# Kernel optimization log

Measured on AMD Instinct MI355X. Metric: run time of the kernel, lower is better.

Reference implementation:

```python
import jax, jax.numpy as jnp
import numpy as np

B, L, S, DIM, NH = 4, 1024, 1024, 1024, 16
DH = DIM // NH


def setup_inputs() -> dict:
    key = jax.random.key(0)
    ks = jax.random.split(key, 16)
    std = 0.02
    inp = {
        'q': jax.random.normal(ks[0], (B, L, DIM), jnp.float32),
        'k': jax.random.normal(ks[1], (B, S, DIM), jnp.float32),
        'v': jax.random.normal(ks[2], (B, S, DIM), jnp.float32),
        'attn_mask': jax.random.bernoulli(ks[3], 0.9, (B, L, S)),
        'pos_bias': jax.random.normal(ks[4], (B, NH, L, S), jnp.float32),
        'Wq': jax.random.normal(ks[5], (DIM, DIM), jnp.float32) * std,
        'bq': jnp.zeros((DIM,), jnp.float32),
        'Wk': jax.random.normal(ks[6], (DIM, DIM), jnp.float32) * std,
        'bk': jnp.zeros((DIM,), jnp.float32),
        'Wv': jax.random.normal(ks[7], (DIM, DIM), jnp.float32) * std,
        'bv': jnp.zeros((DIM,), jnp.float32),
        'Wp': jax.random.normal(ks[8], (DIM, DIM), jnp.float32) * std,
        'bp': jnp.zeros((DIM,), jnp.float32),
        'is_causal': 1,
    }
    return inp


def _attention(q, k, v, attn_mask, pos_bias, Wq, bq, Wk, bk, Wv, bv, Wp, bp, is_causal):
    b, l, _ = q.shape
    s = k.shape[1]
    qh = (q @ Wq + bq).reshape(b, l, NH, DH)   # (B,L,nH,dh)
    kh = (k @ Wk + bk).reshape(b, s, NH, DH)
    vh = (v @ Wv + bv).reshape(b, s, NH, DH)

    mask = attn_mask  # (B,L,S) bool
    if is_causal:
        causal = jnp.tril(jnp.ones((l, l), dtype=bool))
        causal = jnp.pad(causal, ((0, 0), (s - l, 0)), constant_values=True)  # (L,S)
        mask = mask & causal[None]
    # rows with no allowed key attend everywhere (matches torch row-fix)
    row_any = mask.any(axis=-1, keepdims=True)
    mask = jnp.where(row_any, mask, True)

    bias = jnp.where(mask[:, None, :, :], pos_bias, -jnp.inf)  # (B,nH,L,S)
    scale = 1.0 / np.sqrt(DH).astype(np.float32)
    scores = jnp.einsum('blhd,bshd->bhls', qh, kh) * scale + bias
    attn = jax.nn.softmax(scores, axis=-1)
    o = jnp.einsum('bhls,bshd->blhd', attn, vh).reshape(b, l, NH * DH)
    return o @ Wp + bp


def reference(q, k, v, attn_mask, pos_bias, Wq, bq, Wk, bk, Wv, bv, Wp, bp, is_causal):
    return _attention(q, k, v, attn_mask, pos_bias, Wq, bq, Wk, bk, Wv, bv, Wp, bp, is_causal)
```

## Files before the change

kernel.cpp:

```cpp
#include <hip/hip_runtime.h>
#include <hip/hip_bf16.h>

typedef __hip_bfloat16 bf16;
typedef __attribute__((ext_vector_type(4))) float  floatx4;
typedef __attribute__((ext_vector_type(8))) short  short8;
typedef __attribute__((ext_vector_type(8))) __bf16 bf16x8;

constexpr int Bc = 4, Lc = 1024, Sc = 1024, DIMc = 1024, NHc = 16, DHc = 64;

template <typename V>
__device__ auto mfma_bf16_sel(V a, V b, floatx4 c, int)
    -> decltype(__builtin_amdgcn_mfma_f32_16x16x32_bf16(a, b, c, 0, 0, 0)) {
  return __builtin_amdgcn_mfma_f32_16x16x32_bf16(a, b, c, 0, 0, 0);
}
template <typename V>
__device__ floatx4 mfma_bf16_sel(V a, V b, floatx4 c, long) {
  bf16x8 a2 = __builtin_bit_cast(bf16x8, a);
  bf16x8 b2 = __builtin_bit_cast(bf16x8, b);
  return __builtin_amdgcn_mfma_f32_16x16x32_bf16(a2, b2, c, 0, 0, 0);
}
__device__ inline floatx4 mfma_bf16(short8 a, short8 b, floatx4 c) {
  return mfma_bf16_sel(a, b, c, 0);
}

union U8 { uint4 u; bf16 h[8]; };

__device__ inline U8 cvt8(float4 f0, float4 f1) {
    U8 t;
    t.h[0] = __float2bfloat16(f0.x); t.h[1] = __float2bfloat16(f0.y);
    t.h[2] = __float2bfloat16(f0.z); t.h[3] = __float2bfloat16(f0.w);
    t.h[4] = __float2bfloat16(f1.x); t.h[5] = __float2bfloat16(f1.y);
    t.h[6] = __float2bfloat16(f1.z); t.h[7] = __float2bfloat16(f1.w);
    return t;
}

__global__ __launch_bounds__(256)
void prep_kernel(const float* __restrict__ Wq, const float* __restrict__ Wk,
                 const float* __restrict__ Wv, const float* __restrict__ Wp,
                 const int* __restrict__ mask, const int* __restrict__ is_causal_p,
                 bf16* __restrict__ wqt, bf16* __restrict__ wkt,
                 bf16* __restrict__ wvt, bf16* __restrict__ wpt,
                 unsigned long long* __restrict__ mbits,
                 int* __restrict__ rowany_g)
{
    __shared__ float tile[64][68];
    const int tid = threadIdx.x;
    int blk = blockIdx.x;

    if (blk < 1024) {
        const int w  = blk >> 8, t2 = blk & 255;
        const float* W  = (w == 0) ? Wq : (w == 1) ? Wk : (w == 2) ? Wv : Wp;
        bf16*        Wt = (w == 0) ? wqt : (w == 1) ? wkt : (w == 2) ? wvt : wpt;
        const int tk = (t2 >> 4) << 6;
        const int tn = (t2 & 15) << 6;
        #pragma unroll
        for (int i = 0; i < 4; ++i) {
            const int r = (tid >> 4) + i * 16;
            const int c = (tid & 15) << 2;
            *(float4*)(&tile[r][c]) =
                *(const float4*)(W + (size_t)(tk + r) * DIMc + tn + c);
        }
        __syncthreads();
        #pragma unroll
        for (int j = 0; j < 2; ++j) {
            const int nn = tid >> 2;
            const int kc = (tid & 3) + j * 4;
            U8 o;
            #pragma unroll
            for (int u = 0; u < 8; ++u)
                o.h[u] = __float2bfloat16(tile[kc * 8 + u][nn]);
            *(uint4*)(Wt + (size_t)(tn + nn) * DIMc + tk + kc * 8) = o.u;
        }
    } else {
        const int mb  = blk - 1024;
        const int rIb = tid >> 4;
        const int w   = tid & 15;
        const int row = mb * 16 + rIb;
        const int l   = row & (Lc - 1);
        const bool causal = (is_causal_p[0] != 0);

        const int4* mr4 = (const int4*)(mask + (size_t)row * Sc + w * 64);
        unsigned long long bits = 0ull;
        #pragma unroll
        for (int i = 0; i < 16; ++i) {
            int4 m4 = mr4[i];
            unsigned long long nib =
                (unsigned long long)((m4.x != 0) | ((m4.y != 0) << 1) |
                                     ((m4.z != 0) << 2) | ((m4.w != 0) << 3));
            bits |= nib << (4 * i);
        }
        mbits[(size_t)row * 16 + w] = bits;

        const int limit = causal ? l : (Sc - 1);
        const int base  = w * 64;
        unsigned long long am;
        if (limit >= base + 63)  am = bits;
        else if (limit < base)   am = 0ull;
        else                     am = bits & ((2ull << (limit - base)) - 1ull);
        unsigned long long red = am;
        #pragma unroll
        for (int d2 = 1; d2 < 16; d2 <<= 1) red |= __shfl_xor(red, d2);
        if (w == 0) rowany_g[row] = (red != 0ull) ? 1 : 0;
    }
}

constexpr int GPAD = 72;

__global__ __launch_bounds__(256)
void gemm_qkv_kernel(const float* __restrict__ q, const float* __restrict__ k,
                     const float* __restrict__ v,
                     const bf16* __restrict__ wqt, const bf16* __restrict__ wkt,
                     const bf16* __restrict__ wvt,
                     const float* __restrict__ bq, const float* __restrict__ bk,
                     const float* __restrict__ bv,
                     bf16* __restrict__ qh, bf16* __restrict__ kh,
                     bf16* __restrict__ vt)
{
    __shared__ bf16 As[128 * GPAD];
    __shared__ bf16 Bs[128 * GPAD];

    const int z = blockIdx.z;
    const float* A    = (z == 0) ? q   : (z == 1) ? k   : v;
    const bf16*  Bt   = (z == 0) ? wqt : (z == 1) ? wkt : wvt;
    const float* bias = (z == 0) ? bq  : (z == 1) ? bk  : bv;
    bf16*        out  = (z == 0) ? qh  : (z == 1) ? kh  : vt;

    const int tid  = threadIdx.x;
    const int wave = tid >> 6;
    const int lane = tid & 63;
    const int n = lane & 15, g = lane >> 4;
    const int m0 = blockIdx.x * 128;
    const int n0 = blockIdx.y * 128;
    const int wq_m = (wave & 1) * 64, wq_n = (wave >> 1) * 64;

    floatx4 acc[4][4];
    #pragma unroll
    for (int a = 0; a < 4; ++a)
        #pragma unroll
        for (int b2 = 0; b2 < 4; ++b2)
            acc[a][b2] = (floatx4){0.f, 0.f, 0.f, 0.f};

    const int srow   = tid >> 3;
    const int schunk = (tid & 7) * 8;

    float4 a0[4], a1[4]; uint4 bR[4];
    #pragma unroll
    for (int i = 0; i < 4; ++i) {
        const float* ap = A + (size_t)(m0 + srow + i * 32) * DIMc + schunk;
        a0[i] = ((const float4*)ap)[0];
        a1[i] = ((const float4*)ap)[1];
        bR[i] = *(const uint4*)(Bt + (size_t)(n0 + srow + i * 32) * DIMc + schunk);
    }

    for (int k0 = 0; k0 < DIMc; k0 += 64) {
        __syncthreads();
        #pragma unroll
        for (int i = 0; i < 4; ++i) {
            const int r = srow + i * 32;
            U8 t = cvt8(a0[i], a1[i]);
            *(uint4*)(&As[r * GPAD + schunk]) = t.u;
            *(uint4*)(&Bs[r * GPAD + schunk]) = bR[i];
        }
        __syncthreads();
        if (k0 + 64 < DIMc) {
            #pragma unroll
            for (int i = 0; i < 4; ++i) {
                const float* ap =
                    A + (size_t)(m0 + srow + i * 32) * DIMc + k0 + 64 + schunk;
                a0[i] = ((const float4*)ap)[0];
                a1[i] = ((const float4*)ap)[1];
                bR[i] = *(const uint4*)(Bt + (size_t)(n0 + srow + i * 32) * DIMc +
                                        k0 + 64 + schunk);
            }
        }
        #pragma unroll
        for (int ks = 0; ks < 2; ++ks) {
            short8 af[4], bf_[4];
            #pragma unroll
            for (int t = 0; t < 4; ++t) {
                af[t]  = *(const short8*)(&As[(wq_m + t * 16 + n) * GPAD + ks * 32 + g * 8]);
                bf_[t] = *(const short8*)(&Bs[(wq_n + t * 16 + n) * GPAD + ks * 32 + g * 8]);
            }
            #pragma unroll
            for (int tm = 0; tm < 4; ++tm)
                #pragma unroll
                for (int tn = 0; tn < 4; ++tn)
                    acc[tm][tn] = mfma_bf16(af[tm], bf_[tn], acc[tm][tn]);
        }
    }

    #pragma unroll
    for (int tn = 0; tn < 4; ++tn) {
        const int col = n0 + wq_n + tn * 16 + n;
        const float bval = bias[col];
        #pragma unroll
        for (int tm = 0; tm < 4; ++tm) {
            #pragma unroll
            for (int r = 0; r < 4; ++r) {
                const int row = m0 + wq_m + tm * 16 + g * 4 + r;
                const float vv = acc[tm][tn][r] + bval;
                const int bb = row >> 10, ll = row & (Lc - 1);
                const int hh = col >> 6,  dd = col & 63;
                size_t idx;
                if (z < 2) idx = (((size_t)(bb * NHc + hh) * Lc + ll) * DHc) + dd;
                else       idx = (((size_t)(bb * NHc + hh) * DHc + dd) * Sc) + ll;
                out[idx] = __float2bfloat16(vv);
            }
        }
    }
}

__global__ __launch_bounds__(256)
void gemm_out_kernel(const bf16* __restrict__ A, const bf16* __restrict__ Bt,
                     const float* __restrict__ bias, float* __restrict__ out)
{
    __shared__ bf16 As[128 * GPAD];
    __shared__ bf16 Bs[128 * GPAD];

    const int tid  = threadIdx.x;
    const int wave = tid >> 6;
    const int lane = tid & 63;
    const int n = lane & 15, g = lane >> 4;
    const int m0 = blockIdx.x * 128;
    const int n0 = blockIdx.y * 128;
    const int wq_m = (wave & 1) * 64, wq_n = (wave >> 1) * 64;

    floatx4 acc[4][4];
    #pragma unroll
    for (int a = 0; a < 4; ++a)
        #pragma unroll
        for (int b2 = 0; b2 < 4; ++b2)
            acc[a][b2] = (floatx4){0.f, 0.f, 0.f, 0.f};

    const int srow   = tid >> 3;
    const int schunk = (tid & 7) * 8;

    uint4 aR[4], bR[4];
    #pragma unroll
    for (int i = 0; i < 4; ++i) {
        aR[i] = *(const uint4*)(A  + (size_t)(m0 + srow + i * 32) * DIMc + schunk);
        bR[i] = *(const uint4*)(Bt + (size_t)(n0 + srow + i * 32) * DIMc + schunk);
    }

    for (int k0 = 0; k0 < DIMc; k0 += 64) {
        __syncthreads();
        #pragma unroll
        for (int i = 0; i < 4; ++i) {
            const int r = srow + i * 32;
            *(uint4*)(&As[r * GPAD + schunk]) = aR[i];
            *(uint4*)(&Bs[r * GPAD + schunk]) = bR[i];
        }
        __syncthreads();
        if (k0 + 64 < DIMc) {
            #pragma unroll
            for (int i = 0; i < 4; ++i) {
                aR[i] = *(const uint4*)(A  + (size_t)(m0 + srow + i * 32) * DIMc +
                                        k0 + 64 + schunk);
                bR[i] = *(const uint4*)(Bt + (size_t)(n0 + srow + i * 32) * DIMc +
                                        k0 + 64 + schunk);
            }
        }
        #pragma unroll
        for (int ks = 0; ks < 2; ++ks) {
            short8 af[4], bf_[4];
            #pragma unroll
            for (int t = 0; t < 4; ++t) {
                af[t]  = *(const short8*)(&As[(wq_m + t * 16 + n) * GPAD + ks * 32 + g * 8]);
                bf_[t] = *(const short8*)(&Bs[(wq_n + t * 16 + n) * GPAD + ks * 32 + g * 8]);
            }
            #pragma unroll
            for (int tm = 0; tm < 4; ++tm)
                #pragma unroll
                for (int tn = 0; tn < 4; ++tn)
                    acc[tm][tn] = mfma_bf16(af[tm], bf_[tn], acc[tm][tn]);
        }
    }

    #pragma unroll
    for (int tn = 0; tn < 4; ++tn) {
        const int col = n0 + wq_n + tn * 16 + n;
        const float bval = bias[col];
        #pragma unroll
        for (int tm = 0; tm < 4; ++tm) {
            #pragma unroll
            for (int r = 0; r < 4; ++r) {
                const int row = m0 + wq_m + tm * 16 + g * 4 + r;
                out[(size_t)row * DIMc + col] = acc[tm][tn][r] + bval;
            }
        }
    }
}

constexpr int PADk = 72;

__global__ __launch_bounds__(256)
void flash_attn_kernel(const bf16* __restrict__ qh, const bf16* __restrict__ kh,
                       const bf16* __restrict__ vt,
                       const unsigned long long* __restrict__ mbits,
                       const int* __restrict__ rowany_g,
                       const float* __restrict__ pos_bias,
                       const int* __restrict__ is_causal_p, bf16* __restrict__ o)
{
    __shared__ bf16 Ks[64 * PADk];
    __shared__ bf16 Vs[64 * PADk];
    __shared__ bf16 Pw[4][16 * PADk];
    __shared__ int rowany[64];
    __shared__ int hasfix_s;

    const int tid  = threadIdx.x;
    const int lane = tid & 63;
    const int wave = tid >> 6;
    const int n = lane & 15;
    const int g = lane >> 4;

    const int qt = 15 - (blockIdx.x >> 6);
    const int bh = blockIdx.x & 63;
    const int h  = bh & (NHc - 1);
    const int b  = bh >> 4;
    const int l0 = qt * 64;
    const bool causal = (is_causal_p[0] != 0);

    if (tid == 0) hasfix_s = 0;
    __syncthreads();
    if (tid < 64) {
        const int ra = rowany_g[(b << 10) + l0 + tid];
        rowany[tid] = ra;
        if (ra == 0) atomicOr(&hasfix_s, 1);
    }
    __syncthreads();
    const bool hasfix = (hasfix_s != 0);

    const int qrow_frag = l0 + wave * 16 + n;
    const bf16* qp = qh + ((size_t)bh * Lc + qrow_frag) * DHc;
    const short8 qf0 = *(const short8*)(qp + g * 8);
    const short8 qf1 = *(const short8*)(qp + 32 + g * 8);

    const int e0 = tid * 8,        r0a = e0 >> 6, c0a = e0 & 63;
    const int e1 = tid * 8 + 2048, r0b = e1 >> 6, c0b = e1 & 63;
    const bf16* kb0p = kh + ((size_t)bh * Sc + r0a) * DHc + c0a;
    const bf16* kb1p = kh + ((size_t)bh * Sc + r0b) * DHc + c0b;
    const bf16* vb0p = vt + ((size_t)bh * DHc + r0a) * Sc + c0a;
    const bf16* vb1p = vt + ((size_t)bh * DHc + r0b) * Sc + c0b;
    bf16* ksw0 = Ks + r0a * PADk + c0a;
    bf16* ksw1 = Ks + r0b * PADk + c0b;
    bf16* vsw0 = Vs + r0a * PADk + c0a;
    bf16* vsw1 = Vs + r0b * PADk + c0b;

    union F4 { float4 v; float f[4]; };
    const float* brow[4];
    const unsigned long long* mrow[4];
    int limit_r[4]; bool fix_r[4];
    #pragma unroll
    for (int r = 0; r < 4; ++r) {
        const int row = wave * 16 + g * 4 + r;
        const int l = l0 + row;
        brow[r] = pos_bias + ((size_t)bh * Lc + l) * Sc + 4 * n;
        mrow[r] = mbits + ((size_t)(b << 10) + l) * 16;
        limit_r[r] = causal ? l : (Sc - 1);
        fix_r[r] = (rowany[row] == 0);
    }

    floatx4 oacc[4];
    #pragma unroll
    for (int t = 0; t < 4; ++t) oacc[t] = (floatx4){0.f, 0.f, 0.f, 0.f};
    float m_run[4], l_run[4];
    #pragma unroll
    for (int r = 0; r < 4; ++r) { m_run[r] = -3.0e38f; l_run[r] = 0.f; }

    int nchunk = Sc / 64;
    if (causal && !hasfix) nchunk = qt + 1;

    uint4 kr0 = *(const uint4*)(kb0p);
    uint4 kr1 = *(const uint4*)(kb1p);
    uint4 vr0 = *(const uint4*)(vb0p);
    uint4 vr1 = *(const uint4*)(vb1p);
    F4 bcur[4], bnxt[4];
    unsigned long long mcur[4], mnxt[4];
    #pragma unroll
    for (int r = 0; r < 4; ++r) {
        bcur[r].v = *(const float4*)(brow[r]);
        mcur[r]   = mrow[r][0];
    }

    for (int c = 0; c < nchunk; ++c) {
        __syncthreads();
        *(uint4*)ksw0 = kr0;  *(uint4*)ksw1 = kr1;
        *(uint4*)vsw0 = vr0;  *(uint4*)vsw1 = vr1;
        __syncthreads();

        if (c + 1 < nchunk) {
            const size_t ko = (size_t)(c + 1) * 4096;
            const int    vo = (c + 1) * 64;
            kr0 = *(const uint4*)(kb0p + ko);
            kr1 = *(const uint4*)(kb1p + ko);
            vr0 = *(const uint4*)(vb0p + vo);
            vr1 = *(const uint4*)(vb1p + vo);
            #pragma unroll
            for (int r = 0; r < 4; ++r) {
                bnxt[r].v = *(const float4*)(brow[r] + vo);
                mnxt[r]   = mrow[r][c + 1];
            }
        }

        const int s0 = c * 64;

        floatx4 scv[4];
        #pragma unroll
        for (int t = 0; t < 4; ++t) scv[t] = (floatx4){0.f, 0.f, 0.f, 0.f};
        #pragma unroll
        for (int t = 0; t < 4; ++t) {
            const bf16* kp = Ks + (4 * n + t) * PADk + g * 8;
            short8 kb0 = *(const short8*)(kp);
            short8 kb1 = *(const short8*)(kp + 32);
            scv[t] = mfma_bf16(qf0, kb0, scv[t]);
            scv[t] = mfma_bf16(qf1, kb1, scv[t]);
        }

        #pragma unroll
        for (int r = 0; r < 4; ++r) {
            const int row = wave * 16 + g * 4 + r;
            const int nib = (int)((mcur[r] >> (4 * n)) & 15ull);
            float vals[4];
            #pragma unroll
            for (int t = 0; t < 4; ++t) {
                const int s = s0 + 4 * n + t;
                const bool ok = fix_r[r] || (s <= limit_r[r] && ((nib >> t) & 1));
                vals[t] = ok ? scv[t][r] * 0.125f + bcur[r].f[t] : -3.0e38f;
            }
            float cm = fmaxf(fmaxf(vals[0], vals[1]), fmaxf(vals[2], vals[3]));
            cm = fmaxf(cm, __shfl_xor(cm, 1));
            cm = fmaxf(cm, __shfl_xor(cm, 2));
            cm = fmaxf(cm, __shfl_xor(cm, 4));
            cm = fmaxf(cm, __shfl_xor(cm, 8));
            const float mnew = fmaxf(m_run[r], cm);
            const float alpha = __expf(m_run[r] - mnew);
            float csum = 0.f;
            union PK { uint2 u; bf16 hb[4]; } pk;
            #pragma unroll
            for (int t = 0; t < 4; ++t) {
                const float p = (vals[t] < -1.0e37f) ? 0.f : __expf(vals[t] - mnew);
                csum += p;
                pk.hb[t] = __float2bfloat16(p);
            }
            *(uint2*)(&Pw[wave][(row & 15) * PADk + 4 * n]) = pk.u;
            csum += __shfl_xor(csum, 1);
            csum += __shfl_xor(csum, 2);
            csum += __shfl_xor(csum, 4);
            csum += __shfl_xor(csum, 8);
            l_run[r] = l_run[r] * alpha + csum;
            m_run[r] = mnew;
            #pragma unroll
            for (int t = 0; t < 4; ++t) oacc[t][r] *= alpha;
        }

        #pragma unroll
        for (int sc2 = 0; sc2 < 2; ++sc2) {
            short8 pa = *(const short8*)(Pw[wave] + n * PADk + sc2 * 32 + g * 8);
            #pragma unroll
            for (int t = 0; t < 4; ++t) {
                short8 vb = *(const short8*)(Vs + (16 * t + n) * PADk + sc2 * 32 + g * 8);
                oacc[t] = mfma_bf16(pa, vb, oacc[t]);
            }
        }

        #pragma unroll
        for (int r = 0; r < 4; ++r) { bcur[r] = bnxt[r]; mcur[r] = mnxt[r]; }
    }

    #pragma unroll
    for (int r = 0; r < 4; ++r) {
        const int l = l0 + wave * 16 + g * 4 + r;
        const float inv = 1.f / l_run[r];
        #pragma unroll
        for (int t = 0; t < 4; ++t) {
            const int d = 16 * t + n;
            o[((size_t)(b * Lc + l)) * DIMc + h * DHc + d] =
                __float2bfloat16(oacc[t][r] * inv);
        }
    }
}

extern "C" void kernel_launch(void* const* d_in, const int* in_sizes, int n_in,
                              void* d_out, int out_size, void* d_ws, size_t ws_size,
                              hipStream_t stream)
{
    (void)in_sizes; (void)n_in; (void)out_size; (void)ws_size;

    const float* q        = (const float*)d_in[0];
    const float* k        = (const float*)d_in[1];
    const float* v        = (const float*)d_in[2];
    const int*   mask     = (const int*)d_in[3];
    const float* pos_bias = (const float*)d_in[4];
    const float* Wq = (const float*)d_in[5];
    const float* bq = (const float*)d_in[6];
    const float* Wk = (const float*)d_in[7];
    const float* bk = (const float*)d_in[8];
    const float* Wv = (const float*)d_in[9];
    const float* bv = (const float*)d_in[10];
    const float* Wp = (const float*)d_in[11];
    const float* bp = (const float*)d_in[12];
    const int*   is_causal = (const int*)d_in[13];

    const size_t per = (size_t)Bc * NHc * Lc * DHc;
    const size_t wsz = (size_t)DIMc * DIMc;
    bf16* qh  = (bf16*)d_ws;
    bf16* kh  = qh + per;
    bf16* vt  = kh + per;
    bf16* oh  = vt + per;
    bf16* wqt = oh + per;
    bf16* wkt = wqt + wsz;
    bf16* wvt = wkt + wsz;
    bf16* wpt = wvt + wsz;
    unsigned long long* mbits = (unsigned long long*)(wpt + wsz);
    int* rowany_g = (int*)(mbits + (size_t)Bc * Lc * 16);
    float* outp = (float*)d_out;

    dim3 bb(256);

    prep_kernel<<<1280, bb, 0, stream>>>(Wq, Wk, Wv, Wp, mask, is_causal,
                                         wqt, wkt, wvt, wpt, mbits, rowany_g);

    dim3 gq(32, 8, 3);
    gemm_qkv_kernel<<<gq, bb, 0, stream>>>(q, k, v, wqt, wkt, wvt,
                                           bq, bk, bv, qh, kh, vt);

    flash_attn_kernel<<<(Bc * NHc) * (Lc / 64), bb, 0, stream>>>(
        qh, kh, vt, mbits, rowany_g, pos_bias, is_causal, oh);

    dim3 gg(32, 8);
    gemm_out_kernel<<<gg, bb, 0, stream>>>(oh, wpt, bp, outp);
}
```

Before: 601.7 us.

## Pre-convert QKV inputs to bf16, use direct global-to-LDS loads, fold scale into Q

The prep kernel now converts q, k and v from fp32 to bf16 in a separate pass, so the QKV GEMM can stream bf16 tiles straight into LDS with global_load_lds instead of staging them through registers. Both GEMMs drop the padded LDS layout and the register prefetch in favour of direct async LDS fills with a sync after compute. The 1/sqrt(dh) scale moves into the Q projection epilogue, the attention scores start from the positional bias in the MFMA accumulator, and s_setprio is raised around the MFMA blocks. The trade-offs are an extra round trip of the inputs through global memory, the loss of load/compute overlap in the GEMMs, and possible LDS bank conflicts from the unpadded layout.

```diff
diff --git a/kernel.cpp b/kernel.cpp
--- a/kernel.cpp
+++ b/kernel.cpp
@@ -23,9 +23,17 @@
   return mfma_bf16_sel(a, b, c, 0);
 }
 
+__device__ inline void gload16(const bf16* g, bf16* l) {
+  __builtin_amdgcn_global_load_lds(
+      (const __attribute__((address_space(1))) unsigned int*)g,
+      (__attribute__((address_space(3))) unsigned int*)l, 16, 0, 0);
+}
+
 union U8 { uint4 u; bf16 h[8]; };
 
-__device__ inline U8 cvt8(float4 f0, float4 f1) {
+__device__ inline U8 load8cvt(const float* p) {
+    float4 f0 = ((const float4*)p)[0];
+    float4 f1 = ((const float4*)p)[1];
     U8 t;
     t.h[0] = __float2bfloat16(f0.x); t.h[1] = __float2bfloat16(f0.y);
     t.h[2] = __float2bfloat16(f0.z); t.h[3] = __float2bfloat16(f0.w);
@@ -35,9 +43,13 @@
 }
 
 __global__ __launch_bounds__(256)
-void prep_kernel(const float* __restrict__ Wq, const float* __restrict__ Wk,
+void prep_kernel(const float* __restrict__ q, const float* __restrict__ k,
+                 const float* __restrict__ v,
+                 const float* __restrict__ Wq, const float* __restrict__ Wk,
                  const float* __restrict__ Wv, const float* __restrict__ Wp,
                  const int* __restrict__ mask, const int* __restrict__ is_causal_p,
+                 bf16* __restrict__ qb, bf16* __restrict__ kb,
+                 bf16* __restrict__ vb,
                  bf16* __restrict__ wqt, bf16* __restrict__ wkt,
                  bf16* __restrict__ wvt, bf16* __restrict__ wpt,
                  unsigned long long* __restrict__ mbits,
@@ -47,7 +59,14 @@
     const int tid = threadIdx.x;
     int blk = blockIdx.x;
 
-    if (blk < 1024) {
+    if (blk < 6144) {
+        const float* src = (blk < 2048) ? q : (blk < 4096) ? k : v;
+        bf16*        dst = (blk < 2048) ? qb : (blk < 4096) ? kb : vb;
+        const int off = (blk & 2047) * 2048 + tid * 8;
+        U8 t = load8cvt(src + off);
+        *(uint4*)(dst + off) = t.u;
+    } else if (blk < 7168) {
+        blk -= 6144;
         const int w  = blk >> 8, t2 = blk & 255;
         const float* W  = (w == 0) ? Wq : (w == 1) ? Wk : (w == 2) ? Wv : Wp;
         bf16*        Wt = (w == 0) ? wqt : (w == 1) ? wkt : (w == 2) ? wvt : wpt;
@@ -72,7 +91,7 @@
             *(uint4*)(Wt + (size_t)(tn + nn) * DIMc + tk + kc * 8) = o.u;
         }
     } else {
-        const int mb  = blk - 1024;
+        const int mb  = blk - 7168;
         const int rIb = tid >> 4;
         const int w   = tid & 15;
         const int row = mb * 16 + rIb;
@@ -104,11 +123,9 @@
     }
 }
 
-constexpr int GPAD = 72;
-
 __global__ __launch_bounds__(256)
-void gemm_qkv_kernel(const float* __restrict__ q, const float* __restrict__ k,
-                     const float* __restrict__ v,
+void gemm_qkv_kernel(const bf16* __restrict__ qb, const bf16* __restrict__ kb,
+                     const bf16* __restrict__ vb,
                      const bf16* __restrict__ wqt, const bf16* __restrict__ wkt,
                      const bf16* __restrict__ wvt,
                      const float* __restrict__ bq, const float* __restrict__ bk,
@@ -116,14 +133,15 @@
                      bf16* __restrict__ qh, bf16* __restrict__ kh,
                      bf16* __restrict__ vt)
 {
-    __shared__ bf16 As[128 * GPAD];
-    __shared__ bf16 Bs[128 * GPAD];
+    __shared__ __align__(16) bf16 As[128 * 64];
+    __shared__ __align__(16) bf16 Bs[128 * 64];
 
     const int z = blockIdx.z;
-    const float* A    = (z == 0) ? q   : (z == 1) ? k   : v;
+    const bf16*  A    = (z == 0) ? qb  : (z == 1) ? kb  : vb;
     const bf16*  Bt   = (z == 0) ? wqt : (z == 1) ? wkt : wvt;
     const float* bias = (z == 0) ? bq  : (z == 1) ? bk  : bv;
     bf16*        out  = (z == 0) ? qh  : (z == 1) ? kh  : vt;
+    const float  scale = (z == 0) ? 0.125f : 1.0f;
 
     const int tid  = threadIdx.x;
     const int wave = tid >> 6;
@@ -133,6 +151,9 @@
     const int n0 = blockIdx.y * 128;
     const int wq_m = (wave & 1) * 64, wq_n = (wave >> 1) * 64;
 
+    const int lrow   = lane >> 3;
+    const int lchunk = (lane & 7) * 8;
+
     floatx4 acc[4][4];
     #pragma unroll
     for (int a = 0; a < 4; ++a)
@@ -140,46 +161,22 @@
         for (int b2 = 0; b2 < 4; ++b2)
             acc[a][b2] = (floatx4){0.f, 0.f, 0.f, 0.f};
 
-    const int srow   = tid >> 3;
-    const int schunk = (tid & 7) * 8;
-
-    float4 a0[4], a1[4]; uint4 bR[4];
-    #pragma unroll
-    for (int i = 0; i < 4; ++i) {
-        const float* ap = A + (size_t)(m0 + srow + i * 32) * DIMc + schunk;
-        a0[i] = ((const float4*)ap)[0];
-        a1[i] = ((const float4*)ap)[1];
-        bR[i] = *(const uint4*)(Bt + (size_t)(n0 + srow + i * 32) * DIMc + schunk);
-    }
-
     for (int k0 = 0; k0 < DIMc; k0 += 64) {
-        __syncthreads();
-        #pragma unroll
-        for (int i = 0; i < 4; ++i) {
-            const int r = srow + i * 32;
-            U8 t = cvt8(a0[i], a1[i]);
-            *(uint4*)(&As[r * GPAD + schunk]) = t.u;
-            *(uint4*)(&Bs[r * GPAD + schunk]) = bR[i];
-        }
-        __syncthreads();
-        if (k0 + 64 < DIMc) {
-            #pragma unroll
-            for (int i = 0; i < 4; ++i) {
-                const float* ap =
-                    A + (size_t)(m0 + srow + i * 32) * DIMc + k0 + 64 + schunk;
-                a0[i] = ((const float4*)ap)[0];
-                a1[i] = ((const float4*)ap)[1];
-                bR[i] = *(const uint4*)(Bt + (size_t)(n0 + srow + i * 32) * DIMc +
-                                        k0 + 64 + schunk);
-            }
-        }
+        #pragma unroll
+        for (int j = 0; j < 4; ++j) {
+            const int rbase = j * 32 + wave * 8;
+            const int r = rbase + lrow;
+            gload16(A  + (size_t)(m0 + r) * DIMc + k0 + lchunk, As + rbase * 64);
+            gload16(Bt + (size_t)(n0 + r) * DIMc + k0 + lchunk, Bs + rbase * 64);
+        }
+        __syncthreads();
         #pragma unroll
         for (int ks = 0; ks < 2; ++ks) {
             short8 af[4], bf_[4];
             #pragma unroll
             for (int t = 0; t < 4; ++t) {
-                af[t]  = *(const short8*)(&As[(wq_m + t * 16 + n) * GPAD + ks * 32 + g * 8]);
-                bf_[t] = *(const short8*)(&Bs[(wq_n + t * 16 + n) * GPAD + ks * 32 + g * 8]);
+                af[t]  = *(const short8*)(&As[(wq_m + t * 16 + n) * 64 + ks * 32 + g * 8]);
+                bf_[t] = *(const short8*)(&Bs[(wq_n + t * 16 + n) * 64 + ks * 32 + g * 8]);
             }
             #pragma unroll
             for (int tm = 0; tm < 4; ++tm)
@@ -187,6 +184,7 @@
                 for (int tn = 0; tn < 4; ++tn)
                     acc[tm][tn] = mfma_bf16(af[tm], bf_[tn], acc[tm][tn]);
         }
+        __syncthreads();
     }
 
     #pragma unroll
@@ -198,7 +196,7 @@
             #pragma unroll
             for (int r = 0; r < 4; ++r) {
                 const int row = m0 + wq_m + tm * 16 + g * 4 + r;
-                const float vv = acc[tm][tn][r] + bval;
+                const float vv = (acc[tm][tn][r] + bval) * scale;
                 const int bb = row >> 10, ll = row & (Lc - 1);
                 const int hh = col >> 6,  dd = col & 63;
                 size_t idx;
@@ -214,8 +212,8 @@
 void gemm_out_kernel(const bf16* __restrict__ A, const bf16* __restrict__ Bt,
                      const float* __restrict__ bias, float* __restrict__ out)
 {
-    __shared__ bf16 As[128 * GPAD];
-    __shared__ bf16 Bs[128 * GPAD];
+    __shared__ __align__(16) bf16 As[128 * 64];
+    __shared__ __align__(16) bf16 Bs[128 * 64];
 
     const int tid  = threadIdx.x;
     const int wave = tid >> 6;
@@ -225,6 +223,9 @@
     const int n0 = blockIdx.y * 128;
     const int wq_m = (wave & 1) * 64, wq_n = (wave >> 1) * 64;
 
+    const int lrow   = lane >> 3;
+    const int lchunk = (lane & 7) * 8;
+
     floatx4 acc[4][4];
     #pragma unroll
     for (int a = 0; a < 4; ++a)
@@ -232,41 +233,22 @@
         for (int b2 = 0; b2 < 4; ++b2)
             acc[a][b2] = (floatx4){0.f, 0.f, 0.f, 0.f};
 
-    const int srow   = tid >> 3;
-    const int schunk = (tid & 7) * 8;
-
-    uint4 aR[4], bR[4];
-    #pragma unroll
-    for (int i = 0; i < 4; ++i) {
-        aR[i] = *(const uint4*)(A  + (size_t)(m0 + srow + i * 32) * DIMc + schunk);
-        bR[i] = *(const uint4*)(Bt + (size_t)(n0 + srow + i * 32) * DIMc + schunk);
-    }
-
     for (int k0 = 0; k0 < DIMc; k0 += 64) {
-        __syncthreads();
-        #pragma unroll
-        for (int i = 0; i < 4; ++i) {
-            const int r = srow + i * 32;
-            *(uint4*)(&As[r * GPAD + schunk]) = aR[i];
-            *(uint4*)(&Bs[r * GPAD + schunk]) = bR[i];
-        }
-        __syncthreads();
-        if (k0 + 64 < DIMc) {
-            #pragma unroll
-            for (int i = 0; i < 4; ++i) {
-                aR[i] = *(const uint4*)(A  + (size_t)(m0 + srow + i * 32) * DIMc +
-                                        k0 + 64 + schunk);
-                bR[i] = *(const uint4*)(Bt + (size_t)(n0 + srow + i * 32) * DIMc +
-                                        k0 + 64 + schunk);
-            }
-        }
+        #pragma unroll
+        for (int j = 0; j < 4; ++j) {
+            const int rbase = j * 32 + wave * 8;
+            const int r = rbase + lrow;
+            gload16(A  + (size_t)(m0 + r) * DIMc + k0 + lchunk, As + rbase * 64);
+            gload16(Bt + (size_t)(n0 + r) * DIMc + k0 + lchunk, Bs + rbase * 64);
+        }
+        __syncthreads();
         #pragma unroll
         for (int ks = 0; ks < 2; ++ks) {
             short8 af[4], bf_[4];
             #pragma unroll
             for (int t = 0; t < 4; ++t) {
-                af[t]  = *(const short8*)(&As[(wq_m + t * 16 + n) * GPAD + ks * 32 + g * 8]);
-                bf_[t] = *(const short8*)(&Bs[(wq_n + t * 16 + n) * GPAD + ks * 32 + g * 8]);
+                af[t]  = *(const short8*)(&As[(wq_m + t * 16 + n) * 64 + ks * 32 + g * 8]);
+                bf_[t] = *(const short8*)(&Bs[(wq_n + t * 16 + n) * 64 + ks * 32 + g * 8]);
             }
             #pragma unroll
             for (int tm = 0; tm < 4; ++tm)
@@ -274,6 +256,7 @@
                 for (int tn = 0; tn < 4; ++tn)
                     acc[tm][tn] = mfma_bf16(af[tm], bf_[tn], acc[tm][tn]);
         }
+        __syncthreads();
     }
 
     #pragma unroll
@@ -406,7 +389,10 @@
 
         floatx4 scv[4];
         #pragma unroll
-        for (int t = 0; t < 4; ++t) scv[t] = (floatx4){0.f, 0.f, 0.f, 0.f};
+        for (int t = 0; t < 4; ++t)
+            scv[t] = (floatx4){bcur[0].f[t], bcur[1].f[t],
+                               bcur[2].f[t], bcur[3].f[t]};
+        __builtin_amdgcn_s_setprio(1);
         #pragma unroll
         for (int t = 0; t < 4; ++t) {
             const bf16* kp = Ks + (4 * n + t) * PADk + g * 8;
@@ -415,6 +401,7 @@
             scv[t] = mfma_bf16(qf0, kb0, scv[t]);
             scv[t] = mfma_bf16(qf1, kb1, scv[t]);
         }
+        __builtin_amdgcn_s_setprio(0);
 
         #pragma unroll
         for (int r = 0; r < 4; ++r) {
@@ -425,7 +412,7 @@
             for (int t = 0; t < 4; ++t) {
                 const int s = s0 + 4 * n + t;
                 const bool ok = fix_r[r] || (s <= limit_r[r] && ((nib >> t) & 1));
-                vals[t] = ok ? scv[t][r] * 0.125f + bcur[r].f[t] : -3.0e38f;
+                vals[t] = ok ? scv[t][r] : -3.0e38f;
             }
             float cm = fmaxf(fmaxf(vals[0], vals[1]), fmaxf(vals[2], vals[3]));
             cm = fmaxf(cm, __shfl_xor(cm, 1));
@@ -453,6 +440,7 @@
             for (int t = 0; t < 4; ++t) oacc[t][r] *= alpha;
         }
 
+        __builtin_amdgcn_s_setprio(1);
         #pragma unroll
         for (int sc2 = 0; sc2 < 2; ++sc2) {
             short8 pa = *(const short8*)(Pw[wave] + n * PADk + sc2 * 32 + g * 8);
@@ -462,6 +450,7 @@
                 oacc[t] = mfma_bf16(pa, vb, oacc[t]);
             }
         }
+        __builtin_amdgcn_s_setprio(0);
 
         #pragma unroll
         for (int r = 0; r < 4; ++r) { bcur[r] = bnxt[r]; mcur[r] = mnxt[r]; }
@@ -507,7 +496,10 @@
     bf16* kh  = qh + per;
     bf16* vt  = kh + per;
     bf16* oh  = vt + per;
-    bf16* wqt = oh + per;
+    bf16* qb  = oh + per;
+    bf16* kb  = qb + per;
+    bf16* vb  = kb + per;
+    bf16* wqt = vb + per;
     bf16* wkt = wqt + wsz;
     bf16* wvt = wkt + wsz;
     bf16* wpt = wvt + wsz;
@@ -517,11 +509,12 @@
 
     dim3 bb(256);
 
-    prep_kernel<<<1280, bb, 0, stream>>>(Wq, Wk, Wv, Wp, mask, is_causal,
-                                         wqt, wkt, wvt, wpt, mbits, rowany_g);
+    prep_kernel<<<7424, bb, 0, stream>>>(q, k, v, Wq, Wk, Wv, Wp, mask, is_causal,
+                                         qb, kb, vb, wqt, wkt, wvt, wpt,
+                                         mbits, rowany_g);
 
     dim3 gq(32, 8, 3);
-    gemm_qkv_kernel<<<gq, bb, 0, stream>>>(q, k, v, wqt, wkt, wvt,
+    gemm_qkv_kernel<<<gq, bb, 0, stream>>>(qb, kb, vb, wqt, wkt, wvt,
                                            bq, bk, bv, qh, kh, vt);
 
     flash_attn_kernel<<<(Bc * NHc) * (Lc / 64), bb, 0, stream>>>(
```

Result: faster. 551.3 us (-8.4%).
